# Optimization experiments

Hardware: AMD Instinct MI355X
Metric: run time of the kernel (lower is better)

Reference implementation:

```python
import jax, jax.numpy as jnp
import numpy as np
from jax import lax

N_QUBITS = 4
N_QLAYERS = 2
C64 = jnp.complex64
PAIRS = [(i, j) for i in range(N_QUBITS) for j in range(i + 1, N_QUBITS)]  # 6 entangling pairs
CNOT = jnp.array([[1, 0, 0, 0], [0, 1, 0, 0], [0, 0, 0, 1], [0, 0, 1, 0]], dtype=C64)


def _rx(t):
    c = jnp.cos(t / 2).astype(C64)
    s = (-1j * jnp.sin(t / 2)).astype(C64)
    return jnp.stack([jnp.stack([c, s]), jnp.stack([s, c])])


def _ry(t):
    c = jnp.cos(t / 2).astype(C64)
    s = jnp.sin(t / 2).astype(C64)
    return jnp.stack([jnp.stack([c, -s]), jnp.stack([s, c])])


def _rz(t):
    e = jnp.exp(-1j * t.astype(C64) / 2)
    z = jnp.zeros_like(e)
    return jnp.stack([jnp.stack([e, z]), jnp.stack([z, jnp.conj(e)])])


def _apply_1q(state, M, w):
    # state: (B,2,2,2,2); M: (2,2) shared or (B,2,2) per-sample
    s = jnp.moveaxis(state, 1 + w, -1)
    if M.ndim == 2:
        s = jnp.einsum('b...j,ij->b...i', s, M)
    else:
        s = jnp.einsum('b...j,bij->b...i', s, M)
    return jnp.moveaxis(s, -1, 1 + w)


def _apply_2q(state, M4, c, t):
    # M4: (4,4) acting on (wire c, wire t)
    s = jnp.moveaxis(state, (1 + c, 1 + t), (-2, -1))
    sh = s.shape
    s = s.reshape(sh[:-2] + (4,))
    s = jnp.einsum('b...j,ij->b...i', s, M4)
    s = s.reshape(sh)
    return jnp.moveaxis(s, (-2, -1), (1 + c, 1 + t))


def _quantum_batched(angles, q_params):
    # angles: (B, 4) classical outputs; encoding is RY(angles*pi)
    B = angles.shape[0]
    state = jnp.zeros((B, 16), C64).at[:, 0].set(1.0).reshape(B, 2, 2, 2, 2)
    theta = angles * jnp.float32(np.pi)
    c = jnp.cos(theta / 2).astype(C64)  # (B,4)
    s = jnp.sin(theta / 2).astype(C64)
    for w in range(N_QUBITS):
        M = jnp.stack([jnp.stack([c[:, w], -s[:, w]], -1),
                       jnp.stack([s[:, w], c[:, w]], -1)], -2)  # (B,2,2)
        state = _apply_1q(state, M, w)
    per_layer = 3 * N_QUBITS + len(PAIRS)  # 18
    for l in range(N_QLAYERS):
        start = l * per_layer
        rot = q_params[start:start + 3 * N_QUBITS].reshape(N_QUBITS, 3)
        ent = q_params[start + 3 * N_QUBITS:start + per_layer]
        for q in range(N_QUBITS):
            M = _rz(rot[q, 2]) @ _ry(rot[q, 1]) @ _rx(rot[q, 0])
            state = _apply_1q(state, M, q)
        for k, (i, j) in enumerate(PAIRS):
            M4 = jnp.kron(jnp.eye(2, dtype=C64), _rz(ent[k])) @ CNOT  # CNOT then RZ on target
            state = _apply_2q(state, M4, i, j)
    probs = jnp.abs(state) ** 2  # (B,2,2,2,2)
    signs = jnp.array([1.0, -1.0], jnp.float32)
    zs = []
    for w in range(N_QUBITS):
        pw = jnp.moveaxis(probs, 1 + w, -1).reshape(B, -1, 2)
        zs.append((pw.sum(1) * signs).sum(-1))
    return jnp.stack(zs, -1)  # (B,4) PauliZ expvals


def _conv(x, w, b):
    y = lax.conv_general_dilated(x, w, (1, 1), ((1, 1), (1, 1)),
                                 dimension_numbers=('NCHW', 'OIHW', 'NCHW'))
    return y + b[None, :, None, None]


def _pool(x):
    return lax.reduce_window(x, -jnp.inf, lax.max, (1, 1, 2, 2), (1, 1, 2, 2), 'VALID')


def setup_inputs() -> dict:
    key = jax.random.key(0)
    ks = jax.random.split(key, 10)
    B = 4096
    return {
        'x': jax.random.normal(ks[0], (B, 1, 28, 28), jnp.float32),
        'conv1_w': jax.random.normal(ks[1], (16, 1, 3, 3), jnp.float32) * 0.1,
        'conv1_b': jax.random.normal(ks[2], (16,), jnp.float32) * 0.1,
        'conv2_w': jax.random.normal(ks[3], (32, 16, 3, 3), jnp.float32) * 0.05,
        'conv2_b': jax.random.normal(ks[4], (32,), jnp.float32) * 0.1,
        'dense_w': jax.random.normal(ks[5], (4, 1568), jnp.float32) * 0.02,
        'dense_b': jax.random.normal(ks[6], (4,), jnp.float32) * 0.1,
        'q_params': jax.random.normal(ks[7], (36,), jnp.float32) * 0.1,
        'post_w': jax.random.normal(ks[8], (10, 4), jnp.float32) * 0.5,
        'post_b': jax.random.normal(ks[9], (10,), jnp.float32) * 0.1,
    }


def reference(x, conv1_w, conv1_b, conv2_w, conv2_b, dense_w, dense_b, q_params, post_w, post_b):
    h = jax.nn.relu(_conv(x, conv1_w, conv1_b))
    h = _pool(h)
    h = jax.nn.relu(_conv(h, conv2_w, conv2_b))
    h = _pool(h)  # (B,32,7,7)
    h = h.reshape(h.shape[0], 32 * 7 * 7)
    # dropout is identity in eval mode
    angles = h @ dense_w.T + dense_b  # (B,4)
    z = _quantum_batched(angles, q_params)  # (B,4)
    return z @ post_w.T + post_b  # (B,10)
```

## Files before the change

### kernel.cpp

```cpp
#include <hip/hip_runtime.h>

#define PI_F 3.14159265358979323846f

typedef _Float16 half2v __attribute__((ext_vector_type(2)));
typedef _Float16 half4v __attribute__((ext_vector_type(4)));
typedef _Float16 half8v __attribute__((ext_vector_type(8)));
typedef float f32x4 __attribute__((ext_vector_type(4)));

struct C2 { float x, y; };
__device__ __forceinline__ C2 cmul(C2 a, C2 b) {
    return C2{a.x * b.x - a.y * b.y, a.x * b.y + a.y * b.x};
}

__device__ __forceinline__ void gate1(float& re, float& im, int l, int w,
                                      C2 m00, C2 m01, C2 m10, C2 m11) {
    int mask = 1 << (3 - w);
    float pre = __shfl_xor(re, mask, 64);
    float pim = __shfl_xor(im, mask, 64);
    bool b = (l & mask) != 0;
    C2 d = b ? m11 : m00;
    C2 o = b ? m10 : m01;
    float nre = d.x * re - d.y * im + o.x * pre - o.y * pim;
    float nim = d.x * im + d.y * re + o.x * pim + o.y * pre;
    re = nre; im = nim;
}

#define WS_C1B 2560
#define WS_DWT 2688
#define WS_GROT 8960
#define WS_GENT 9024

__global__ __launch_bounds__(256) void qnn_prep(
    const float* __restrict__ w1g, const float* __restrict__ w2g,
    const float* __restrict__ dwg, const float* __restrict__ qpg,
    float* __restrict__ ws)
{
    int t = threadIdx.x;
    for (int e = t; e < 640; e += 256) {
        int kstep = e >> 7, rem = e & 127;
        int ntile = rem >> 6, lane = rem & 63;
        int kq = lane >> 4, n = lane & 15;
        int oc = ntile * 16 + n;
        int pi = kstep * 2 + (kq >> 1);
        half8v h;
        #pragma unroll
        for (int jj = 0; jj < 8; ++jj) {
            int ic = (kq & 1) * 8 + jj;
            float v = (pi < 9) ? w2g[oc * 144 + ic * 9 + pi] : 0.f;
            h[jj] = (_Float16)v;
        }
        *(float4*)(ws + e * 4) = __builtin_bit_cast(float4, h);
    }
    if (t < 64) {
        int ky = t >> 4, n = t & 15;
        half4v h;
        #pragma unroll
        for (int j = 0; j < 4; ++j) {
            float v = (ky < 3 && j < 3) ? w1g[n * 9 + ky * 3 + j] : 0.f;
            h[j] = (_Float16)v;
        }
        *(float2*)(ws + WS_C1B + t * 2) = __builtin_bit_cast(float2, h);
    }
    for (int e = t; e < 1568; e += 256) {
        float4 v = {dwg[e], dwg[1568 + e], dwg[3136 + e], dwg[4704 + e]};
        *(float4*)(ws + WS_DWT + e * 4) = v;
    }
    if (t < 8) {
        int layer = t >> 2, q = t & 3;
        int st = layer * 18;
        float a0 = qpg[st + 3 * q], a1 = qpg[st + 3 * q + 1], a2 = qpg[st + 3 * q + 2];
        float cx = cosf(0.5f * a0), sx = sinf(0.5f * a0);
        float cy = cosf(0.5f * a1), sy = sinf(0.5f * a1);
        float cz = cosf(0.5f * a2), sz = sinf(0.5f * a2);
        C2 T00{cy * cx,  sy * sx}, T01{-sy * cx, -cy * sx};
        C2 T10{sy * cx, -cy * sx}, T11{ cy * cx, -sy * sx};
        C2 E0{cz, -sz}, E1{cz, sz};
        C2 m00 = cmul(E0, T00), m01 = cmul(E0, T01);
        C2 m10 = cmul(E1, T10), m11 = cmul(E1, T11);
        float* gm = ws + WS_GROT + t * 8;
        gm[0] = m00.x; gm[1] = m00.y; gm[2] = m01.x; gm[3] = m01.y;
        gm[4] = m10.x; gm[5] = m10.y; gm[6] = m11.x; gm[7] = m11.y;
    }
    if (t >= 32 && t < 44) {
        int k = t - 32;
        float e = qpg[(k / 6) * 18 + 12 + (k % 6)];
        ws[WS_GENT + k * 2]     = cosf(0.5f * e);
        ws[WS_GENT + k * 2 + 1] = sinf(0.5f * e);
    }
}

__global__ __launch_bounds__(256, 6) void qnn_fused(
    const float* __restrict__ xg,
    const float* __restrict__ b1g, const float* __restrict__ b2g,
    const float* __restrict__ dbg,
    const float* __restrict__ wsc,
    const float* __restrict__ pwg, const float* __restrict__ pbg,
    float* __restrict__ out)
{
    const int b = blockIdx.x;
    const int t = threadIdx.x;
    const int lane = t & 63;
    const int wv = __builtin_amdgcn_readfirstlane(t >> 6);
    const int kq = lane >> 4;
    const int lm = lane & 15;

    __shared__ __align__(16) unsigned xhl[930];
    __shared__ __align__(16) _Float16 p1f[16 * 20 * 16];
    __shared__ __align__(16) float angp[16];

    half8v bC2[5][2];
    {
        const float4* wsB = (const float4*)wsc;
        #pragma unroll
        for (int ks = 0; ks < 5; ++ks)
            #pragma unroll
            for (int nt = 0; nt < 2; ++nt)
                bC2[ks][nt] = __builtin_bit_cast(half8v, wsB[(ks * 2 + nt) * 64 + lane]);
    }
    half4v bC1 = __builtin_bit_cast(half4v, *(const float2*)(wsc + WS_C1B + lane * 2));
    float bias1 = b1g[lm];
    float b20 = b2g[lm], b21 = b2g[16 + lm];

    const float* xb = xg + (size_t)b * 784;
    for (int j = t; j < 900; j += 256) {
        int y = j / 30, x = j - y * 30;
        float v = 0.f;
        if (y >= 1 && y <= 28 && x >= 1 && x <= 28)
            v = xb[(y - 1) * 28 + (x - 1)];
        _Float16 h = (_Float16)v;
        _Float16 l = (_Float16)(v - (float)h);
        half2v p; p.x = h; p.y = l;
        xhl[j] = __builtin_bit_cast(unsigned, p);
    }
    if (t < 30) xhl[900 + t] = 0u;
    {
        uint4 z4 = {0u, 0u, 0u, 0u};
        uint4* p4 = (uint4*)p1f;
        #pragma unroll
        for (int j = 0; j < 3; ++j) {
            int i = t + j * 256;
            if (i < 640) p4[i] = z4;
        }
    }
    __syncthreads();

    {
        int kyc = (kq < 3) ? kq : 0;
        int pos = lm & 3;
        int pyo = pos >> 1, pxo = pos & 1;
        int p14 = wv * 4 + (lm >> 2);
        int Y = p14 / 14, X = p14 - Y * 14;
        int q14 = wv * 4 + kq;
        int r = q14 / 14, c = q14 - r * 14;
        for (int tile = wv; tile < 49; tile += 4) {
            int py = 2 * Y + pyo, px = 2 * X + pxo;
            int base = (py + kyc) * 30 + px;
            unsigned u0 = xhl[base], u1 = xhl[base + 1], u2 = xhl[base + 2], u3 = xhl[base + 3];
            half2v h0 = __builtin_bit_cast(half2v, u0);
            half2v h1 = __builtin_bit_cast(half2v, u1);
            half2v h2 = __builtin_bit_cast(half2v, u2);
            half2v h3 = __builtin_bit_cast(half2v, u3);
            half4v ah = {h0.x, h1.x, h2.x, h3.x};
            half4v al = {h0.y, h1.y, h2.y, h3.y};
            f32x4 acc = {bias1, bias1, bias1, bias1};
            acc = __builtin_amdgcn_mfma_f32_16x16x16f16(ah, bC1, acc, 0, 0, 0);
            acc = __builtin_amdgcn_mfma_f32_16x16x16f16(al, bC1, acc, 0, 0, 0);
            float v = fmaxf(fmaxf(acc.x, acc.y), fmaxf(acc.z, acc.w));
            v = fmaxf(v, 0.f);
            p1f[((r + 1) * 20 + (c + 1)) * 16 + lm] = (_Float16)v;
            X += 2; Y += 1; if (X >= 14) { X -= 14; Y += 1; }
            c += 2; r += 1; if (c >= 14) { c -= 14; r += 1; }
        }
    }
    __syncthreads();

    {
        float dp0 = 0.f, dp1 = 0.f, dp2 = 0.f, dp3 = 0.f;
        const float4* dt = (const float4*)(wsc + WS_DWT);
        for (int tile = wv; tile < 13; tile += 4) {
            int m = tile * 16 + lm;
            int quad = m >> 2; if (quad > 48) quad = 48;
            int pos = m & 3;
            int Y = quad / 7, X = quad - Y * 7;
            int py = 2 * Y + (pos >> 1), px = 2 * X + (pos & 1);
            int base0 = py * 20 + px;
            f32x4 acc0 = {b20, b20, b20, b20};
            f32x4 acc1 = {b21, b21, b21, b21};
            int ich = (kq & 1) * 8;
            #pragma unroll
            for (int ks = 0; ks < 5; ++ks) {
                int pi = ks * 2 + (kq >> 1);
                if (pi > 8) pi = 8;
                int ky = (pi >= 6) ? 2 : ((pi >= 3) ? 1 : 0);
                int kx = pi - ky * 3;
                half8v a = *(const half8v*)(&p1f[(base0 + ky * 20 + kx) * 16 + ich]);
                acc0 = __builtin_amdgcn_mfma_f32_16x16x32_f16(a, bC2[ks][0], acc0, 0, 0, 0);
                acc1 = __builtin_amdgcn_mfma_f32_16x16x32_f16(a, bC2[ks][1], acc1, 0, 0, 0);
            }
            int quadO = tile * 4 + kq;
            if (quadO < 49) {
                float v0 = fmaxf(fmaxf(fmaxf(acc0.x, acc0.y), fmaxf(acc0.z, acc0.w)), 0.f);
                float v1 = fmaxf(fmaxf(fmaxf(acc1.x, acc1.y), fmaxf(acc1.z, acc1.w)), 0.f);
                float4 q0 = dt[lm * 49 + quadO];
                float4 q1 = dt[(16 + lm) * 49 + quadO];
                dp0 = fmaf(v0, q0.x, fmaf(v1, q1.x, dp0));
                dp1 = fmaf(v0, q0.y, fmaf(v1, q1.y, dp1));
                dp2 = fmaf(v0, q0.z, fmaf(v1, q1.z, dp2));
                dp3 = fmaf(v0, q0.w, fmaf(v1, q1.w, dp3));
            }
        }
        #pragma unroll
        for (int m = 32; m >= 1; m >>= 1) {
            dp0 += __shfl_xor(dp0, m, 64);
            dp1 += __shfl_xor(dp1, m, 64);
            dp2 += __shfl_xor(dp2, m, 64);
            dp3 += __shfl_xor(dp3, m, 64);
        }
        if (lane == 0) {
            float4 dpv = {dp0, dp1, dp2, dp3};
            *(float4*)&angp[wv * 4] = dpv;
        }
    }
    __syncthreads();

    if (t < 64) {
        float4 a0v = *(const float4*)&angp[0];
        float4 a1v = *(const float4*)&angp[4];
        float4 a2v = *(const float4*)&angp[8];
        float4 a3v = *(const float4*)&angp[12];
        float aw[4] = {a0v.x + a1v.x + a2v.x + a3v.x + dbg[0],
                       a0v.y + a1v.y + a2v.y + a3v.y + dbg[1],
                       a0v.z + a1v.z + a2v.z + a3v.z + dbg[2],
                       a0v.w + a1v.w + a2v.w + a3v.w + dbg[3]};
        int l = t & 15;
        float re = (l == 0) ? 1.f : 0.f;
        float im = 0.f;
        #pragma unroll
        for (int w = 0; w < 4; ++w) {
            float th = aw[w] * (PI_F * 0.5f);
            float c = cosf(th), s = sinf(th);
            gate1(re, im, l, w, C2{c, 0.f}, C2{-s, 0.f}, C2{s, 0.f}, C2{c, 0.f});
        }
        #pragma unroll
        for (int layer = 0; layer < 2; ++layer) {
            #pragma unroll
            for (int q = 0; q < 4; ++q) {
                const float* gm = wsc + WS_GROT + (layer * 4 + q) * 8;
                gate1(re, im, l, q, C2{gm[0], gm[1]}, C2{gm[2], gm[3]},
                                     C2{gm[4], gm[5]}, C2{gm[6], gm[7]});
            }
            const int pi_[6] = {0, 0, 0, 1, 1, 2};
            const int pj_[6] = {1, 2, 3, 2, 3, 3};
            #pragma unroll
            for (int k = 0; k < 6; ++k) {
                int i = pi_[k], j = pj_[k];
                const float* em = wsc + WS_GENT + (layer * 6 + k) * 2;
                float ce = em[0], se = em[1];
                int maskj = 1 << (3 - j);
                float pre = __shfl_xor(re, maskj, 64);
                float pim = __shfl_xor(im, maskj, 64);
                bool bi = ((l >> (3 - i)) & 1) != 0;
                re = bi ? pre : re;
                im = bi ? pim : im;
                bool bj = (l & maskj) != 0;
                C2 ph{ce, bj ? se : -se};
                C2 r = cmul(C2{re, im}, ph);
                re = r.x; im = r.y;
            }
        }
        float pr = re * re + im * im;
        float z0 = ((l >> 3) & 1) ? -pr : pr;
        float z1 = ((l >> 2) & 1) ? -pr : pr;
        float z2 = ((l >> 1) & 1) ? -pr : pr;
        float z3 = (l & 1)        ? -pr : pr;
        #pragma unroll
        for (int m = 1; m <= 8; m <<= 1) {
            z0 += __shfl_xor(z0, m, 64);
            z1 += __shfl_xor(z1, m, 64);
            z2 += __shfl_xor(z2, m, 64);
            z3 += __shfl_xor(z3, m, 64);
        }
        if (t < 10) {
            float4 pw4 = *(const float4*)(pwg + t * 4);
            float o = pbg[t];
            o = fmaf(z0, pw4.x, o); o = fmaf(z1, pw4.y, o);
            o = fmaf(z2, pw4.z, o); o = fmaf(z3, pw4.w, o);
            out[(size_t)b * 10 + t] = o;
        }
    }
}

extern "C" void kernel_launch(void* const* d_in, const int* in_sizes, int n_in,
                              void* d_out, int out_size, void* d_ws, size_t ws_size,
                              hipStream_t stream) {
    const float* x  = (const float*)d_in[0];
    const float* w1 = (const float*)d_in[1];
    const float* b1 = (const float*)d_in[2];
    const float* w2 = (const float*)d_in[3];
    const float* b2 = (const float*)d_in[4];
    const float* dw = (const float*)d_in[5];
    const float* db = (const float*)d_in[6];
    const float* qp = (const float*)d_in[7];
    const float* pw = (const float*)d_in[8];
    const float* pb = (const float*)d_in[9];
    float* out = (float*)d_out;
    float* ws  = (float*)d_ws;
    int B = in_sizes[0] / 784;

    qnn_prep<<<1, 256, 0, stream>>>(w1, w2, dw, qp, ws);
    qnn_fused<<<B, 256, 0, stream>>>(x, b1, b2, db, ws, pw, pb, out);
}
```

Before: 117.7 us.

## Process two images per block to amortize weight loads and reduce padding

Each block now handles two batch images, launching B/2 blocks. Per-lane weight fragments and biases are loaded once and reused for both images. The conv1 and conv2 tile loops interleave work across the images to cut the idle tail iterations. The pooled conv1 buffer row pitch shrinks from 20 to 17 to save shared memory. This assumes B is even, and the doubled shared memory per block may reduce occupancy.

```diff
diff --git a/kernel.cpp b/kernel.cpp
--- a/kernel.cpp
+++ b/kernel.cpp
@@ -24,6 +24,9 @@
     float nim = d.x * im + d.y * re + o.x * pim + o.y * pre;
     re = nre; im = nim;
 }
+
+#define P1C 17
+#define P1_IMG (16 * P1C * 16)
 
 #define WS_C1B 2560
 #define WS_DWT 2688
@@ -104,9 +107,9 @@
     const int kq = lane >> 4;
     const int lm = lane & 15;
 
-    __shared__ __align__(16) unsigned xhl[930];
-    __shared__ __align__(16) _Float16 p1f[16 * 20 * 16];
-    __shared__ __align__(16) float angp[16];
+    __shared__ __align__(16) unsigned xhl[2 * 932];
+    __shared__ __align__(16) _Float16 p1f[2 * P1_IMG];
+    __shared__ __align__(16) float angp[32];
 
     half8v bC2[5][2];
     {
@@ -121,25 +124,26 @@
     float bias1 = b1g[lm];
     float b20 = b2g[lm], b21 = b2g[16 + lm];
 
-    const float* xb = xg + (size_t)b * 784;
-    for (int j = t; j < 900; j += 256) {
-        int y = j / 30, x = j - y * 30;
+    for (int j = t; j < 1800; j += 256) {
+        int img = (j >= 900) ? 1 : 0;
+        int jj = j - img * 900;
+        int y = jj / 30, x = jj - y * 30;
         float v = 0.f;
         if (y >= 1 && y <= 28 && x >= 1 && x <= 28)
-            v = xb[(y - 1) * 28 + (x - 1)];
+            v = xg[(size_t)(2 * b + img) * 784 + (y - 1) * 28 + (x - 1)];
         _Float16 h = (_Float16)v;
         _Float16 l = (_Float16)(v - (float)h);
         half2v p; p.x = h; p.y = l;
-        xhl[j] = __builtin_bit_cast(unsigned, p);
-    }
-    if (t < 30) xhl[900 + t] = 0u;
+        xhl[img * 932 + jj] = __builtin_bit_cast(unsigned, p);
+    }
+    if (t < 64) xhl[(t >> 5) * 932 + 900 + (t & 31)] = 0u;
     {
         uint4 z4 = {0u, 0u, 0u, 0u};
         uint4* p4 = (uint4*)p1f;
         #pragma unroll
-        for (int j = 0; j < 3; ++j) {
+        for (int j = 0; j < 5; ++j) {
             int i = t + j * 256;
-            if (i < 640) p4[i] = z4;
+            if (i < 1088) p4[i] = z4;
         }
     }
     __syncthreads();
@@ -152,10 +156,20 @@
         int Y = p14 / 14, X = p14 - Y * 14;
         int q14 = wv * 4 + kq;
         int r = q14 / 14, c = q14 - r * 14;
-        for (int tile = wv; tile < 49; tile += 4) {
+        const int uB = ((49 - wv + 3) >> 2) * 4 + wv;
+        for (int u = wv; u < 98; u += 4) {
+            if (u == uB) {
+                int p14b = (u - 49) * 4 + (lm >> 2);
+                Y = p14b / 14; X = p14b - Y * 14;
+                int q14b = (u - 49) * 4 + kq;
+                r = q14b / 14; c = q14b - r * 14;
+            }
+            int off = (u >= 49) ? 1 : 0;
+            const unsigned* xh = xhl + off * 932;
+            _Float16* pf = p1f + off * P1_IMG;
             int py = 2 * Y + pyo, px = 2 * X + pxo;
             int base = (py + kyc) * 30 + px;
-            unsigned u0 = xhl[base], u1 = xhl[base + 1], u2 = xhl[base + 2], u3 = xhl[base + 3];
+            unsigned u0 = xh[base], u1 = xh[base + 1], u2 = xh[base + 2], u3 = xh[base + 3];
             half2v h0 = __builtin_bit_cast(half2v, u0);
             half2v h1 = __builtin_bit_cast(half2v, u1);
             half2v h2 = __builtin_bit_cast(half2v, u2);
@@ -167,7 +181,7 @@
             acc = __builtin_amdgcn_mfma_f32_16x16x16f16(al, bC1, acc, 0, 0, 0);
             float v = fmaxf(fmaxf(acc.x, acc.y), fmaxf(acc.z, acc.w));
             v = fmaxf(v, 0.f);
-            p1f[((r + 1) * 20 + (c + 1)) * 16 + lm] = (_Float16)v;
+            pf[((r + 1) * P1C + (c + 1)) * 16 + lm] = (_Float16)v;
             X += 2; Y += 1; if (X >= 14) { X -= 14; Y += 1; }
             c += 2; r += 1; if (c >= 14) { c -= 14; r += 1; }
         }
@@ -175,25 +189,29 @@
     __syncthreads();
 
     {
-        float dp0 = 0.f, dp1 = 0.f, dp2 = 0.f, dp3 = 0.f;
+        float dpA0 = 0.f, dpA1 = 0.f, dpA2 = 0.f, dpA3 = 0.f;
+        float dpB0 = 0.f, dpB1 = 0.f, dpB2 = 0.f, dpB3 = 0.f;
         const float4* dt = (const float4*)(wsc + WS_DWT);
-        for (int tile = wv; tile < 13; tile += 4) {
+        int ich = (kq & 1) * 8;
+        for (int u = wv; u < 26; u += 4) {
+            int imgB = (u >= 13);
+            int tile = u - (imgB ? 13 : 0);
+            const _Float16* pf = p1f + (imgB ? P1_IMG : 0);
             int m = tile * 16 + lm;
             int quad = m >> 2; if (quad > 48) quad = 48;
             int pos = m & 3;
             int Y = quad / 7, X = quad - Y * 7;
             int py = 2 * Y + (pos >> 1), px = 2 * X + (pos & 1);
-            int base0 = py * 20 + px;
+            int base0 = py * P1C + px;
             f32x4 acc0 = {b20, b20, b20, b20};
             f32x4 acc1 = {b21, b21, b21, b21};
-            int ich = (kq & 1) * 8;
             #pragma unroll
             for (int ks = 0; ks < 5; ++ks) {
                 int pi = ks * 2 + (kq >> 1);
                 if (pi > 8) pi = 8;
                 int ky = (pi >= 6) ? 2 : ((pi >= 3) ? 1 : 0);
                 int kx = pi - ky * 3;
-                half8v a = *(const half8v*)(&p1f[(base0 + ky * 20 + kx) * 16 + ich]);
+                half8v a = *(const half8v*)(&pf[(base0 + ky * P1C + kx) * 16 + ich]);
                 acc0 = __builtin_amdgcn_mfma_f32_16x16x32_f16(a, bC2[ks][0], acc0, 0, 0, 0);
                 acc1 = __builtin_amdgcn_mfma_f32_16x16x32_f16(a, bC2[ks][1], acc1, 0, 0, 0);
             }
@@ -203,31 +221,41 @@
                 float v1 = fmaxf(fmaxf(fmaxf(acc1.x, acc1.y), fmaxf(acc1.z, acc1.w)), 0.f);
                 float4 q0 = dt[lm * 49 + quadO];
                 float4 q1 = dt[(16 + lm) * 49 + quadO];
-                dp0 = fmaf(v0, q0.x, fmaf(v1, q1.x, dp0));
-                dp1 = fmaf(v0, q0.y, fmaf(v1, q1.y, dp1));
-                dp2 = fmaf(v0, q0.z, fmaf(v1, q1.z, dp2));
-                dp3 = fmaf(v0, q0.w, fmaf(v1, q1.w, dp3));
+                if (!imgB) {
+                    dpA0 = fmaf(v0, q0.x, fmaf(v1, q1.x, dpA0));
+                    dpA1 = fmaf(v0, q0.y, fmaf(v1, q1.y, dpA1));
+                    dpA2 = fmaf(v0, q0.z, fmaf(v1, q1.z, dpA2));
+                    dpA3 = fmaf(v0, q0.w, fmaf(v1, q1.w, dpA3));
+                } else {
+                    dpB0 = fmaf(v0, q0.x, fmaf(v1, q1.x, dpB0));
+                    dpB1 = fmaf(v0, q0.y, fmaf(v1, q1.y, dpB1));
+                    dpB2 = fmaf(v0, q0.z, fmaf(v1, q1.z, dpB2));
+                    dpB3 = fmaf(v0, q0.w, fmaf(v1, q1.w, dpB3));
+                }
             }
         }
         #pragma unroll
         for (int m = 32; m >= 1; m >>= 1) {
-            dp0 += __shfl_xor(dp0, m, 64);
-            dp1 += __shfl_xor(dp1, m, 64);
-            dp2 += __shfl_xor(dp2, m, 64);
-            dp3 += __shfl_xor(dp3, m, 64);
+            dpA0 += __shfl_xor(dpA0, m, 64); dpA1 += __shfl_xor(dpA1, m, 64);
+            dpA2 += __shfl_xor(dpA2, m, 64); dpA3 += __shfl_xor(dpA3, m, 64);
+            dpB0 += __shfl_xor(dpB0, m, 64); dpB1 += __shfl_xor(dpB1, m, 64);
+            dpB2 += __shfl_xor(dpB2, m, 64); dpB3 += __shfl_xor(dpB3, m, 64);
         }
         if (lane == 0) {
-            float4 dpv = {dp0, dp1, dp2, dp3};
-            *(float4*)&angp[wv * 4] = dpv;
+            float4 a4 = {dpA0, dpA1, dpA2, dpA3};
+            float4 b4 = {dpB0, dpB1, dpB2, dpB3};
+            *(float4*)&angp[wv * 4] = a4;
+            *(float4*)&angp[16 + wv * 4] = b4;
         }
     }
     __syncthreads();
 
-    if (t < 64) {
-        float4 a0v = *(const float4*)&angp[0];
-        float4 a1v = *(const float4*)&angp[4];
-        float4 a2v = *(const float4*)&angp[8];
-        float4 a3v = *(const float4*)&angp[12];
+    if (t < 128) {
+        int img = wv;
+        float4 a0v = *(const float4*)&angp[img * 16 + 0];
+        float4 a1v = *(const float4*)&angp[img * 16 + 4];
+        float4 a2v = *(const float4*)&angp[img * 16 + 8];
+        float4 a3v = *(const float4*)&angp[img * 16 + 12];
         float aw[4] = {a0v.x + a1v.x + a2v.x + a3v.x + dbg[0],
                        a0v.y + a1v.y + a2v.y + a3v.y + dbg[1],
                        a0v.z + a1v.z + a2v.z + a3v.z + dbg[2],
@@ -280,12 +308,13 @@
             z2 += __shfl_xor(z2, m, 64);
             z3 += __shfl_xor(z3, m, 64);
         }
-        if (t < 10) {
-            float4 pw4 = *(const float4*)(pwg + t * 4);
-            float o = pbg[t];
+        int ln = t & 63;
+        if (ln < 10) {
+            float4 pw4 = *(const float4*)(pwg + ln * 4);
+            float o = pbg[ln];
             o = fmaf(z0, pw4.x, o); o = fmaf(z1, pw4.y, o);
             o = fmaf(z2, pw4.z, o); o = fmaf(z3, pw4.w, o);
-            out[(size_t)b * 10 + t] = o;
+            out[(size_t)(2 * b + img) * 10 + ln] = o;
         }
     }
 }
@@ -308,5 +337,5 @@
     int B = in_sizes[0] / 784;
 
     qnn_prep<<<1, 256, 0, stream>>>(w1, w2, dw, qp, ws);
-    qnn_fused<<<B, 256, 0, stream>>>(x, b1, b2, db, ws, pw, pb, out);
-}
+    qnn_fused<<<B / 2, 256, 0, stream>>>(x, b1, b2, db, ws, pw, pb, out);
+}
```

Result: slower. 121.0 us (+2.8%).

## Drop hi/lo fp16 split for conv1, repack shared buffers, raise occupancy

Applied to the files above, without the earlier changes.

Conv1 input is now stored as a single fp16 value per pixel, packed in pairs, instead of a hi/lo fp16 split, so conv1 needs one MFMA per tile instead of two. The pooled conv1 output buffer is reorganised into two channel-half planes with a row pitch of 17 pixels, which shrinks shared memory use and changes the bank mapping of conv2 reads. Launch bounds raise the target to 8 blocks per CU. Dropping the low-order fp16 residual lowers the precision of the conv1 input, which could affect accuracy.

```diff
diff --git a/kernel.cpp b/kernel.cpp
--- a/kernel.cpp
+++ b/kernel.cpp
@@ -24,6 +24,9 @@
     float nim = d.x * im + d.y * re + o.x * pim + o.y * pre;
     re = nre; im = nim;
 }
+
+#define P1_PIX 272
+#define P1_SEL (P1_PIX * 8)
 
 #define WS_C1B 2560
 #define WS_DWT 2688
@@ -89,7 +92,7 @@
     }
 }
 
-__global__ __launch_bounds__(256, 6) void qnn_fused(
+__global__ __launch_bounds__(256, 8) void qnn_fused(
     const float* __restrict__ xg,
     const float* __restrict__ b1g, const float* __restrict__ b2g,
     const float* __restrict__ dbg,
@@ -104,8 +107,8 @@
     const int kq = lane >> 4;
     const int lm = lane & 15;
 
-    __shared__ __align__(16) unsigned xhl[930];
-    __shared__ __align__(16) _Float16 p1f[16 * 20 * 16];
+    __shared__ __align__(16) unsigned xp[932];
+    __shared__ __align__(16) _Float16 p1f[2 * P1_SEL];
     __shared__ __align__(16) float angp[16];
 
     half8v bC2[5][2];
@@ -122,24 +125,30 @@
     float b20 = b2g[lm], b21 = b2g[16 + lm];
 
     const float* xb = xg + (size_t)b * 784;
-    for (int j = t; j < 900; j += 256) {
-        int y = j / 30, x = j - y * 30;
-        float v = 0.f;
-        if (y >= 1 && y <= 28 && x >= 1 && x <= 28)
-            v = xb[(y - 1) * 28 + (x - 1)];
-        _Float16 h = (_Float16)v;
-        _Float16 l = (_Float16)(v - (float)h);
-        half2v p; p.x = h; p.y = l;
-        xhl[j] = __builtin_bit_cast(unsigned, p);
-    }
-    if (t < 30) xhl[900 + t] = 0u;
+    {
+        int y = t / 30, x = t - y * 30;
+        for (int i = t; i < 930; i += 256) {
+            bool in1 = (y >= 1 && y <= 28 && x >= 1 && x <= 28);
+            float v1 = in1 ? xb[(y - 1) * 28 + (x - 1)] : 0.f;
+            int y2 = y, x2 = x + 1;
+            if (x2 == 30) { x2 = 0; y2 = y + 1; }
+            bool in2 = (y2 >= 1 && y2 <= 28 && x2 >= 1 && x2 <= 28);
+            float v2 = in2 ? xb[(y2 - 1) * 28 + (x2 - 1)] : 0.f;
+            half2v p;
+            p.x = (_Float16)v1;
+            p.y = (_Float16)v2;
+            xp[i] = __builtin_bit_cast(unsigned, p);
+            x += 16; y += 8; if (x >= 30) { x -= 30; y += 1; }
+        }
+        if (t < 2) xp[930 + t] = 0u;
+    }
     {
         uint4 z4 = {0u, 0u, 0u, 0u};
         uint4* p4 = (uint4*)p1f;
         #pragma unroll
         for (int j = 0; j < 3; ++j) {
             int i = t + j * 256;
-            if (i < 640) p4[i] = z4;
+            if (i < 544) p4[i] = z4;
         }
     }
     __syncthreads();
@@ -155,19 +164,14 @@
         for (int tile = wv; tile < 49; tile += 4) {
             int py = 2 * Y + pyo, px = 2 * X + pxo;
             int base = (py + kyc) * 30 + px;
-            unsigned u0 = xhl[base], u1 = xhl[base + 1], u2 = xhl[base + 2], u3 = xhl[base + 3];
-            half2v h0 = __builtin_bit_cast(half2v, u0);
-            half2v h1 = __builtin_bit_cast(half2v, u1);
-            half2v h2 = __builtin_bit_cast(half2v, u2);
-            half2v h3 = __builtin_bit_cast(half2v, u3);
-            half4v ah = {h0.x, h1.x, h2.x, h3.x};
-            half4v al = {h0.y, h1.y, h2.y, h3.y};
+            uint2 u = {xp[base], xp[base + 2]};
+            half4v a = __builtin_bit_cast(half4v, u);
             f32x4 acc = {bias1, bias1, bias1, bias1};
-            acc = __builtin_amdgcn_mfma_f32_16x16x16f16(ah, bC1, acc, 0, 0, 0);
-            acc = __builtin_amdgcn_mfma_f32_16x16x16f16(al, bC1, acc, 0, 0, 0);
+            acc = __builtin_amdgcn_mfma_f32_16x16x16f16(a, bC1, acc, 0, 0, 0);
             float v = fmaxf(fmaxf(acc.x, acc.y), fmaxf(acc.z, acc.w));
             v = fmaxf(v, 0.f);
-            p1f[((r + 1) * 20 + (c + 1)) * 16 + lm] = (_Float16)v;
+            int pixw = (r + 1) * 17 + (c + 1);
+            p1f[(lm >> 3) * P1_SEL + pixw * 8 + (lm & 7)] = (_Float16)v;
             X += 2; Y += 1; if (X >= 14) { X -= 14; Y += 1; }
             c += 2; r += 1; if (c >= 14) { c -= 14; r += 1; }
         }
@@ -177,23 +181,23 @@
     {
         float dp0 = 0.f, dp1 = 0.f, dp2 = 0.f, dp3 = 0.f;
         const float4* dt = (const float4*)(wsc + WS_DWT);
+        const _Float16* pfs = p1f + (kq & 1) * P1_SEL;
         for (int tile = wv; tile < 13; tile += 4) {
             int m = tile * 16 + lm;
             int quad = m >> 2; if (quad > 48) quad = 48;
             int pos = m & 3;
             int Y = quad / 7, X = quad - Y * 7;
             int py = 2 * Y + (pos >> 1), px = 2 * X + (pos & 1);
-            int base0 = py * 20 + px;
+            int pixb = py * 17 + px;
             f32x4 acc0 = {b20, b20, b20, b20};
             f32x4 acc1 = {b21, b21, b21, b21};
-            int ich = (kq & 1) * 8;
             #pragma unroll
             for (int ks = 0; ks < 5; ++ks) {
                 int pi = ks * 2 + (kq >> 1);
                 if (pi > 8) pi = 8;
                 int ky = (pi >= 6) ? 2 : ((pi >= 3) ? 1 : 0);
                 int kx = pi - ky * 3;
-                half8v a = *(const half8v*)(&p1f[(base0 + ky * 20 + kx) * 16 + ich]);
+                half8v a = *(const half8v*)(&pfs[(pixb + ky * 17 + kx) * 8]);
                 acc0 = __builtin_amdgcn_mfma_f32_16x16x32_f16(a, bC2[ks][0], acc0, 0, 0, 0);
                 acc1 = __builtin_amdgcn_mfma_f32_16x16x32_f16(a, bC2[ks][1], acc1, 0, 0, 0);
             }
```

Result: slower. 142.8 us (+21.3%).
